# Performance work log

Hardware: AMD Instinct MI355X
Metric: run time of the kernel (lower is better)

## Reference

```python
import jax, jax.numpy as jnp
import numpy as np

SINKHORN_ITERS = 10


def _optimal_transport(attn, phi, iters):
    # attn: [N,H,W,W], phi: scalar dustbin score
    bs, h, w, _ = attn.shape
    marginal = jnp.concatenate([jnp.ones((w,), attn.dtype), jnp.array([float(w)], attn.dtype)]) / (2.0 * w)
    log_mu = jnp.log(marginal)  # [W+1], broadcasts over [N,H,W+1]
    log_nu = log_mu
    # augment with dustbin row/col filled with phi -> [N,H,W+1,W+1]
    sim = jnp.concatenate([attn, jnp.broadcast_to(phi, (bs, h, w, 1))], axis=-1)
    sim = jnp.concatenate([sim, jnp.broadcast_to(phi, (bs, h, 1, w + 1))], axis=-2)

    def body(i, uv):
        u, v = uv
        v = log_nu - jax.nn.logsumexp(sim + u[..., :, None], axis=2)
        u = log_mu - jax.nn.logsumexp(sim + v[..., None, :], axis=3)
        return (u, v)

    u0 = jnp.zeros((bs, h, w + 1), attn.dtype)
    u, v = jax.lax.fori_loop(0, iters, body, (u0, u0))
    attn_ot = sim + u[..., :, None] + v[..., None, :]
    return jnp.exp(attn_ot + jnp.log(2.0 * w))


def _compute_low_res_disp(pos_shift, attn, occ_mask=None):
    # attn: [N,H,W,W] (dustbins removed); pos_shift: [W,W]
    w = attn.shape[-1]
    high_response = jnp.argmax(attn, axis=-1)  # [N,H,W]
    response_range = jnp.stack([high_response - 1, high_response, high_response + 1], axis=-1)  # [N,H,W,3]
    attn_pad = jnp.pad(attn, ((0, 0), (0, 0), (0, 0), (1, 1)))
    attn_rw = jnp.take_along_axis(attn_pad, response_range + 1, axis=-1)  # [N,H,W,3]
    norm = attn_rw.sum(-1, keepdims=True)
    norm = jnp.where(norm < 0.1, 1.0, norm)  # occ_mask is None branch
    attn_rw = attn_rw / norm
    pos_pad = jnp.pad(pos_shift, ((0, 0), (1, 1)))  # [W,W+2]
    pos_pad = jnp.broadcast_to(pos_pad[None, None], attn_pad.shape)
    pos_rw = jnp.take_along_axis(pos_pad, response_range + 1, axis=-1)
    disp = (attn_rw * pos_rw).sum(-1)  # [N,H,W]
    return disp, norm


def setup_inputs() -> dict:
    key = jax.random.key(0)
    k1, _ = jax.random.split(key)
    N, H, W = 4, 120, 256
    attn_weight = jax.random.normal(k1, (N, H, W, W), dtype=jnp.float32)
    phi = jnp.zeros((1,), dtype=jnp.float32)
    return {"attn_weight": attn_weight, "phi": phi}


def reference(attn_weight, phi):
    w = attn_weight.shape[2]
    attn_ot = _optimal_transport(attn_weight, phi[0], SINKHORN_ITERS)  # [N,H,W+1,W+1]
    # relative position shift, clamped at 0
    pos = jnp.arange(w, dtype=attn_weight.dtype)
    pos_shift = jnp.maximum(pos[:, None] - pos[None, :], 0.0)  # [W,W]
    disp_pred_low_res, matched_attn = _compute_low_res_disp(pos_shift, attn_ot[..., :-1, :-1], None)
    occ_pred = 1.0 - matched_attn.squeeze(-1)  # [N,H,W]
    return disp_pred_low_res, occ_pred
```

## Files before the change

kernel.cpp:

```cpp
#include <hip/hip_runtime.h>
#include <cstdint>

namespace {

constexpr int W = 256;
constexpr int ITERS = 10;
constexpr int PSTR = 260;

__device__ __forceinline__ float dpp_add_xor1(float x) {
  int y = __builtin_amdgcn_mov_dpp(__float_as_int(x), 0xB1, 0xF, 0xF, true);
  return x + __int_as_float(y);
}
__device__ __forceinline__ float dpp_add_xor2(float x) {
  int y = __builtin_amdgcn_mov_dpp(__float_as_int(x), 0x4E, 0xF, 0xF, true);
  return x + __int_as_float(y);
}
template <int PAT>
__device__ __forceinline__ float swz_add(float x) {
  return x + __int_as_float(__builtin_amdgcn_ds_swizzle(__float_as_int(x), PAT));
}
__device__ __forceinline__ float allred32(float x) {
  x = dpp_add_xor1(x);
  x = dpp_add_xor2(x);
  x = swz_add<0x101F>(x);
  x = swz_add<0x201F>(x);
  x = swz_add<0x401F>(x);
  return x;
}
__device__ __forceinline__ float rcpf(float x) {
  float r;
  asm("v_rcp_f32 %0, %1" : "=v"(r) : "v"(x));
  return r;
}

__global__ __launch_bounds__(1024)
void sinkhorn_disp_kernel(
    const float* __restrict__ attn,
    const float* __restrict__ phi_p,
    float* __restrict__ out,
    int nh)
{
  __shared__ __align__(16) float E_lds[1024 * 32];
  __shared__ __align__(16) float fpart[16][PSTR];
  __shared__ __align__(16) float ev_l[W];
  __shared__ __align__(16) float seup[32];
  __shared__ float evW_s;

  const int tid = threadIdx.x;
  const int tc  = tid & 31;
  const int tr  = tid >> 5;
  const int bid = blockIdx.x;
  const int sw  = tid & 7;
  float* myE = &E_lds[tid * 32];
  #define RDCH(c) (*(const float4*)&myE[4 * ((c) ^ sw)])

  const float ephi  = __expf(phi_p[0]);
  const float inv2w = 1.0f / (2.0f * W);

  const int ch0 = 4 * ((2 * tc) ^ ((tc >> 2) & 7));

  float Er[4][8];
  {
    const float* src = attn + (size_t)bid * (W * W) + (size_t)(tr * 8) * W + tc * 8;
    #pragma unroll
    for (int a = 0; a < 4; ++a) {
      float4 x0 = *(const float4*)(src + a * W);
      float4 x1 = *(const float4*)(src + a * W + 4);
      Er[a][0] = __expf(x0.x); Er[a][1] = __expf(x0.y);
      Er[a][2] = __expf(x0.z); Er[a][3] = __expf(x0.w);
      Er[a][4] = __expf(x1.x); Er[a][5] = __expf(x1.y);
      Er[a][6] = __expf(x1.z); Er[a][7] = __expf(x1.w);
    }
    #pragma unroll
    for (int ap = 0; ap < 4; ++ap) {
      float4 x0 = *(const float4*)(src + (4 + ap) * W);
      float4 x1 = *(const float4*)(src + (4 + ap) * W + 4);
      *(float4*)&myE[4 * ((2 * ap)     ^ sw)] =
          make_float4(__expf(x0.x), __expf(x0.y), __expf(x0.z), __expf(x0.w));
      *(float4*)&myE[4 * ((2 * ap + 1) ^ sw)] =
          make_float4(__expf(x1.x), __expf(x1.y), __expf(x1.z), __expf(x1.w));
    }
  }

  float eul[8];
  #pragma unroll
  for (int a = 0; a < 8; ++a) eul[a] = 1.0f;
  float euW = 1.0f;

  for (int it = 0; it < ITERS; ++it) {
    {
      float cp[8];
      #pragma unroll
      for (int b = 0; b < 8; ++b) cp[b] = 0.0f;
      #pragma unroll
      for (int a = 0; a < 4; ++a) {
        #pragma unroll
        for (int b = 0; b < 8; ++b)
          cp[b] = __builtin_fmaf(Er[a][b], eul[a], cp[b]);
      }
      #pragma unroll
      for (int ap = 0; ap < 4; ++ap) {
        float4 e0 = RDCH(2 * ap), e1 = RDCH(2 * ap + 1);
        float ua = eul[4 + ap];
        cp[0] = __builtin_fmaf(e0.x, ua, cp[0]);
        cp[1] = __builtin_fmaf(e0.y, ua, cp[1]);
        cp[2] = __builtin_fmaf(e0.z, ua, cp[2]);
        cp[3] = __builtin_fmaf(e0.w, ua, cp[3]);
        cp[4] = __builtin_fmaf(e1.x, ua, cp[4]);
        cp[5] = __builtin_fmaf(e1.y, ua, cp[5]);
        cp[6] = __builtin_fmaf(e1.z, ua, cp[6]);
        cp[7] = __builtin_fmaf(e1.w, ua, cp[7]);
      }
      #pragma unroll
      for (int b = 0; b < 8; ++b) cp[b] += __shfl_xor(cp[b], 32, 64);
      if (!(tr & 1)) {
        *(float4*)&fpart[tr >> 1][ch0    ] = make_float4(cp[0], cp[1], cp[2], cp[3]);
        *(float4*)&fpart[tr >> 1][ch0 ^ 4] = make_float4(cp[4], cp[5], cp[6], cp[7]);
      }
      if (tc == 0)
        seup[tr] = ((eul[0] + eul[1]) + (eul[2] + eul[3]))
                 + ((eul[4] + eul[5]) + (eul[6] + eul[7]));
    }
    __syncthreads();
    if (tid < 2 * W) {
      const int j  = tid >> 1;
      const int fj = ((((j >> 2) ^ ((j >> 5) & 7)) << 2) | (j & 3));
      const int g0 = (tid & 1) * 8;
      float s = 0.0f;
      #pragma unroll
      for (int g = 0; g < 8; ++g) s += fpart[g0 + g][fj];
      s = dpp_add_xor1(s);
      if (!(tid & 1)) ev_l[fj] = inv2w * rcpf(s + ephi * euW);
    } else if ((tid >> 6) == 8) {
      float s = allred32(seup[tid & 31]);
      if (tid == 512) evW_s = 0.5f * rcpf(ephi * (s + euW));
    }
    __syncthreads();
    {
      const float evW = evW_s;
      float4 v0 = *(const float4*)&ev_l[ch0];
      float4 v1 = *(const float4*)&ev_l[ch0 ^ 4];
      float vl[8] = {v0.x, v0.y, v0.z, v0.w, v1.x, v1.y, v1.z, v1.w};
      float rp[8];
      #pragma unroll
      for (int a = 0; a < 4; ++a) {
        float s = 0.0f;
        #pragma unroll
        for (int b = 0; b < 8; ++b)
          s = __builtin_fmaf(Er[a][b], vl[b], s);
        rp[a] = s;
      }
      #pragma unroll
      for (int ap = 0; ap < 4; ++ap) {
        float4 e0 = RDCH(2 * ap), e1 = RDCH(2 * ap + 1);
        rp[4 + ap] = e0.x * vl[0] + e0.y * vl[1] + e0.z * vl[2] + e0.w * vl[3]
                   + e1.x * vl[4] + e1.y * vl[5] + e1.z * vl[6] + e1.w * vl[7];
      }
      float sev = ((vl[0] + vl[1]) + (vl[2] + vl[3]))
                + ((vl[4] + vl[5]) + (vl[6] + vl[7]));
      #pragma unroll
      for (int a = 0; a < 8; ++a) rp[a] = allred32(rp[a]);
      sev = allred32(sev);
      const float eAdd = ephi * evW;
      #pragma unroll
      for (int a = 0; a < 8; ++a) eul[a] = inv2w * rcpf(rp[a] + eAdd);
      euW = 0.5f * rcpf(ephi * (sev + evW));
    }
  }

  float vl[8];
  {
    float4 v0 = *(const float4*)&ev_l[ch0];
    float4 v1 = *(const float4*)&ev_l[ch0 ^ 4];
    vl[0] = v0.x; vl[1] = v0.y; vl[2] = v0.z; vl[3] = v0.w;
    vl[4] = v1.x; vl[5] = v1.y; vl[6] = v1.z; vl[7] = v1.w;
  }
  float res_disp = 0.0f, res_occ = 0.0f;
  #pragma unroll
  for (int a = 0; a < 8; ++a) {
    float v[8];
    if (a < 4) {
      #pragma unroll
      for (int b = 0; b < 8; ++b) v[b] = Er[a < 4 ? a : 0][b] * vl[b];
    } else {
      float4 e0 = RDCH(2 * (a - 4)), e1 = RDCH(2 * (a - 4) + 1);
      v[0] = e0.x * vl[0]; v[1] = e0.y * vl[1];
      v[2] = e0.z * vl[2]; v[3] = e0.w * vl[3];
      v[4] = e1.x * vl[4]; v[5] = e1.y * vl[5];
      v[6] = e1.z * vl[6]; v[7] = e1.w * vl[7];
    }
    float m = v[0]; int mj = tc * 8;
    #pragma unroll
    for (int b = 1; b < 8; ++b) {
      if (v[b] > m) { m = v[b]; mj = tc * 8 + b; }
    }
    unsigned long long best =
        (((unsigned long long)__float_as_uint(m)) << 32) |
        (unsigned)(65535 - mj);
    #pragma unroll
    for (int off = 16; off > 0; off >>= 1) {
      unsigned long long o = __shfl_xor(best, off, 32);
      if (o > best) best = o;
    }
    const int jm = 65535 - (int)(best & 0xffffffffull);
    const int i  = tr * 8 + a;
    const float us = eul[a] * (2.0f * W);
    float num = 0.0f, den = 0.0f;
    #pragma unroll
    for (int b = 0; b < 8; ++b) {
      int j = tc * 8 + b;
      if (j >= jm - 1 && j <= jm + 1) {
        float w = v[b] * us;
        den += w;
        num += w * fmaxf((float)(i - j), 0.0f);
      }
    }
    den = allred32(den);
    num = allred32(num);
    if (tc == a) {
      float norm = (den < 0.1f) ? 1.0f : den;
      res_disp = num / norm;
      res_occ  = 1.0f - norm;
    }
  }
  if (tc < 8) {
    const int i = tr * 8 + tc;
    out[(size_t)bid * W + i] = res_disp;
    out[(size_t)nh * W + (size_t)bid * W + i] = res_occ;
  }
  #undef RDCH
}

}

extern "C" void kernel_launch(void* const* d_in, const int* in_sizes, int n_in,
                              void* d_out, int out_size, void* d_ws, size_t ws_size,
                              hipStream_t stream) {
  (void)n_in; (void)d_ws; (void)ws_size; (void)out_size;
  const float* attn = (const float*)d_in[0];
  const float* phi  = (const float*)d_in[1];
  float* out = (float*)d_out;
  const int nh = in_sizes[0] / (W * W);
  sinkhorn_disp_kernel<<<dim3(nh), dim3(1024), 0, stream>>>(attn, phi, out, nh);
}
```

Before: 241.1 us.

## Keep five rows in registers and prefetch the next block's tile into cache

Moves one more row of exp(attn) from LDS into registers (5 register rows, 3 LDS rows), cutting LDS reads per Sinkhorn iteration. It also issues dummy global loads during iterations 2-5 to pull the attn tile for block bid+256 into cache ahead of its launch, aiming to hide load latency for the second wave of blocks. The phi exponent is made wave-uniform via readfirstlane. Extra registers per thread at 1024 threads per block may cause spills, and the prefetch only pays off if the cached lines survive until the later block runs.

Measured after the change: 235.8 us. 1.02x faster.

```diff
diff --git a/kernel.cpp b/kernel.cpp
--- a/kernel.cpp
+++ b/kernel.cpp
@@ -54,16 +54,17 @@
   float* myE = &E_lds[tid * 32];
   #define RDCH(c) (*(const float4*)&myE[4 * ((c) ^ sw)])
 
-  const float ephi  = __expf(phi_p[0]);
+  const float ephi  = __int_as_float(
+      __builtin_amdgcn_readfirstlane(__float_as_int(__expf(phi_p[0]))));
   const float inv2w = 1.0f / (2.0f * W);
 
   const int ch0 = 4 * ((2 * tc) ^ ((tc >> 2) & 7));
 
-  float Er[4][8];
+  float Er[5][8];
   {
     const float* src = attn + (size_t)bid * (W * W) + (size_t)(tr * 8) * W + tc * 8;
     #pragma unroll
-    for (int a = 0; a < 4; ++a) {
+    for (int a = 0; a < 5; ++a) {
       float4 x0 = *(const float4*)(src + a * W);
       float4 x1 = *(const float4*)(src + a * W + 4);
       Er[a][0] = __expf(x0.x); Er[a][1] = __expf(x0.y);
@@ -72,12 +73,12 @@
       Er[a][6] = __expf(x1.z); Er[a][7] = __expf(x1.w);
     }
     #pragma unroll
-    for (int ap = 0; ap < 4; ++ap) {
-      float4 x0 = *(const float4*)(src + (4 + ap) * W);
-      float4 x1 = *(const float4*)(src + (4 + ap) * W + 4);
-      *(float4*)&myE[4 * ((2 * ap)     ^ sw)] =
+    for (int r = 0; r < 3; ++r) {
+      float4 x0 = *(const float4*)(src + (5 + r) * W);
+      float4 x1 = *(const float4*)(src + (5 + r) * W + 4);
+      *(float4*)&myE[4 * ((2 + 2 * r) ^ sw)] =
           make_float4(__expf(x0.x), __expf(x0.y), __expf(x0.z), __expf(x0.w));
-      *(float4*)&myE[4 * ((2 * ap + 1) ^ sw)] =
+      *(float4*)&myE[4 * ((3 + 2 * r) ^ sw)] =
           make_float4(__expf(x1.x), __expf(x1.y), __expf(x1.z), __expf(x1.w));
     }
   }
@@ -88,20 +89,26 @@
   float euW = 1.0f;
 
   for (int it = 0; it < ITERS; ++it) {
+    if (it >= 2 && it <= 5 && bid + 256 < nh) {
+      const float* pf = attn + (size_t)(bid + 256) * (W * W)
+                      + ((size_t)(it - 2) * 1024 + tid) * 16;
+      float x = *pf;
+      asm volatile("" :: "v"(x));
+    }
     {
       float cp[8];
       #pragma unroll
       for (int b = 0; b < 8; ++b) cp[b] = 0.0f;
       #pragma unroll
-      for (int a = 0; a < 4; ++a) {
+      for (int a = 0; a < 5; ++a) {
         #pragma unroll
         for (int b = 0; b < 8; ++b)
           cp[b] = __builtin_fmaf(Er[a][b], eul[a], cp[b]);
       }
       #pragma unroll
-      for (int ap = 0; ap < 4; ++ap) {
-        float4 e0 = RDCH(2 * ap), e1 = RDCH(2 * ap + 1);
-        float ua = eul[4 + ap];
+      for (int r = 0; r < 3; ++r) {
+        float4 e0 = RDCH(2 + 2 * r), e1 = RDCH(3 + 2 * r);
+        float ua = eul[5 + r];
         cp[0] = __builtin_fmaf(e0.x, ua, cp[0]);
         cp[1] = __builtin_fmaf(e0.y, ua, cp[1]);
         cp[2] = __builtin_fmaf(e0.z, ua, cp[2]);
@@ -143,7 +150,7 @@
       float vl[8] = {v0.x, v0.y, v0.z, v0.w, v1.x, v1.y, v1.z, v1.w};
       float rp[8];
       #pragma unroll
-      for (int a = 0; a < 4; ++a) {
+      for (int a = 0; a < 5; ++a) {
         float s = 0.0f;
         #pragma unroll
         for (int b = 0; b < 8; ++b)
@@ -151,10 +158,10 @@
         rp[a] = s;
       }
       #pragma unroll
-      for (int ap = 0; ap < 4; ++ap) {
-        float4 e0 = RDCH(2 * ap), e1 = RDCH(2 * ap + 1);
-        rp[4 + ap] = e0.x * vl[0] + e0.y * vl[1] + e0.z * vl[2] + e0.w * vl[3]
-                   + e1.x * vl[4] + e1.y * vl[5] + e1.z * vl[6] + e1.w * vl[7];
+      for (int r = 0; r < 3; ++r) {
+        float4 e0 = RDCH(2 + 2 * r), e1 = RDCH(3 + 2 * r);
+        rp[5 + r] = e0.x * vl[0] + e0.y * vl[1] + e0.z * vl[2] + e0.w * vl[3]
+                  + e1.x * vl[4] + e1.y * vl[5] + e1.z * vl[6] + e1.w * vl[7];
       }
       float sev = ((vl[0] + vl[1]) + (vl[2] + vl[3]))
                 + ((vl[4] + vl[5]) + (vl[6] + vl[7]));
@@ -179,11 +186,11 @@
   #pragma unroll
   for (int a = 0; a < 8; ++a) {
     float v[8];
-    if (a < 4) {
-      #pragma unroll
-      for (int b = 0; b < 8; ++b) v[b] = Er[a < 4 ? a : 0][b] * vl[b];
+    if (a < 5) {
+      #pragma unroll
+      for (int b = 0; b < 8; ++b) v[b] = Er[a < 5 ? a : 0][b] * vl[b];
     } else {
-      float4 e0 = RDCH(2 * (a - 4)), e1 = RDCH(2 * (a - 4) + 1);
+      float4 e0 = RDCH(2 + 2 * (a - 5)), e1 = RDCH(3 + 2 * (a - 5));
       v[0] = e0.x * vl[0]; v[1] = e0.y * vl[1];
       v[2] = e0.z * vl[2]; v[3] = e0.w * vl[3];
       v[4] = e1.x * vl[4]; v[5] = e1.y * vl[5];
```
